# Kernel optimization log

Measured on AMD Instinct MI355X. Metric: run time of the kernel, lower is better.

## Reference

```python
import jax, jax.numpy as jnp
import numpy as np

GRID_SIZE = 5
SPLINE_ORDER = 3
GRID_RANGE = (-1.0, 1.0)
BATCH, IN_FEATURES, OUT_FEATURES = 8192, 512, 512


def make_grid():
    h = (GRID_RANGE[1] - GRID_RANGE[0]) / GRID_SIZE
    n = GRID_SIZE + 2 * SPLINE_ORDER + 1  # 12 knots
    return jnp.linspace(GRID_RANGE[0] - SPLINE_ORDER * h,
                        GRID_RANGE[1] + SPLINE_ORDER * h,
                        n, dtype=jnp.float32)


def b_spline(x, grid, k=SPLINE_ORDER):
    # Cox-de Boor recursion. x: (B, in) -> basis: (B, in, grid_size + k)
    x = x[..., None]                     # (B, in, 1)
    g = grid[None, None, :]              # (1, 1, n_knots)
    basis = ((x >= g[..., :-1]) & (x < g[..., 1:])).astype(x.dtype)
    for p in range(1, k + 1):
        left_denom = g[..., p:-1] - g[..., :-(p + 1)]
        right_denom = g[..., p + 1:] - g[..., 1:-p]
        left_denom = jnp.where(left_denom > 0, left_denom, jnp.ones_like(left_denom))
        right_denom = jnp.where(right_denom > 0, right_denom, jnp.ones_like(right_denom))
        left = (x - g[..., :-(p + 1)]) / left_denom * basis[..., :-1]
        right = (g[..., p + 1:] - x) / right_denom * basis[..., 1:]
        basis = left + right
    return basis


def setup_inputs() -> dict:
    key = jax.random.key(0)
    k1, k2, k3 = jax.random.split(key, 3)
    # x uniform in grid_range so spline basis is active
    x = jax.random.uniform(k1, (BATCH, IN_FEATURES), jnp.float32, minval=-1.0, maxval=1.0)
    # kaiming_uniform-like init for base weight
    bound = 1.0 / np.sqrt(IN_FEATURES)
    base_weight = jax.random.uniform(k2, (OUT_FEATURES, IN_FEATURES), jnp.float32,
                                     minval=-bound, maxval=bound)
    spline_weight = jax.random.normal(k3, (OUT_FEATURES, IN_FEATURES,
                                           GRID_SIZE + SPLINE_ORDER), jnp.float32) * 0.1
    return {"x": x, "base_weight": base_weight, "spline_weight": spline_weight}


def reference(x, base_weight, spline_weight):
    grid = make_grid()
    scale_base, scale_spline = 1.0, 1.0
    base_out = x @ base_weight.T                         # (B, out)
    basis = b_spline(x, grid, SPLINE_ORDER)              # (B, in, G+k)
    spline_out = jnp.einsum('bil,oil->bo', basis, spline_weight)
    return scale_base * base_out + scale_spline * spline_out
```

## Files before the change

### kernel.cpp

```cpp
#include <hip/hip_runtime.h>
#include <stdint.h>

typedef _Float16 half8 __attribute__((ext_vector_type(8)));
typedef float floatx4 __attribute__((ext_vector_type(4)));
typedef uint32_t u32x4 __attribute__((ext_vector_type(4)));

#define IF 512
#define NF 512
#define KT_TOTAL 72
#define TILE_B 16384
#define B_WS_BYTES ((size_t)KT_TOTAL * 4 * TILE_B)

__device__ __forceinline__ uint32_t swz(uint32_t b) {
  return b ^ (((b >> 7) & 7u) << 4);
}
__device__ __forceinline__ uint32_t pk(float a, float b) {
  return __builtin_bit_cast(uint32_t, __builtin_amdgcn_cvt_pkrtz(a, b));
}

__device__ __forceinline__ u32x4 BASIS8(float xv) {
  float u = (xv + 2.2f) * 2.5f;
  float fj = __builtin_floorf(u);
  fj = fminf(fmaxf(fj, 3.0f), 7.0f);
  float t = u - fj;
  float omt = 1.0f - t;
  float t2 = t * t, t3 = t2 * t;
  float w0 = omt * omt * omt * 0.16666666666666666f;
  float w1 = __builtin_fmaf(0.5f, t3, 0.66666666666666666f - t2);
  float w2 = __builtin_fmaf(0.5f, (t2 - t3) + t, 0.16666666666666666f);
  float w3 = t3 * 0.16666666666666666f;
  uint32_t c0 = pk(w0, w1);
  uint32_t c1 = pk(w2, w3);
  int j3 = (int)fj - 3;
  int sh = j3 << 4;
  uint64_t w = (uint64_t)c0 | ((uint64_t)c1 << 32);
  uint64_t lo = (sh < 64) ? (w << sh) : 0ull;
  uint64_t hi = (sh == 0) ? 0ull : ((sh < 64) ? (w >> (64 - sh)) : w);
  u32x4 r;
  r.x = (uint32_t)lo; r.y = (uint32_t)(lo >> 32);
  r.z = (uint32_t)hi; r.w = (uint32_t)(hi >> 32);
  return r;
}

__global__ __launch_bounds__(256)
void kan_zero(float4* __restrict__ p, int n4) {
  const int stride = gridDim.x * 256;
  for (int i = blockIdx.x * 256 + threadIdx.x; i < n4; i += stride)
    p[i] = (float4){0.f, 0.f, 0.f, 0.f};
}

__global__ __launch_bounds__(256)
void kan_prepB(const float* __restrict__ bwg, const float* __restrict__ swg,
               uint8_t* __restrict__ wsB)
{
  const int gid = blockIdx.x * 256 + threadIdx.x;
  const int T = gid >> 10;
  const int q = gid & 1023;
  const int kt = T >> 2;
  const int nt = T & 3;
  const uint32_t p = swz((uint32_t)q * 16u);
  const int row = p >> 7;
  const int c   = (p & 127) >> 1;
  const int n = nt * 128 + row;
  const float* src = (kt < 8) ? bwg + (size_t)n * IF + kt * 64 + c
                              : swg + (size_t)n * 4096 + (kt - 8) * 64 + c;
  float4 f0 = ((const float4*)src)[0];
  float4 f1 = ((const float4*)src)[1];
  u32x4 v; v.x = pk(f0.x, f0.y); v.y = pk(f0.z, f0.w);
           v.z = pk(f1.x, f1.y); v.w = pk(f1.z, f1.w);
  *(u32x4*)(wsB + (size_t)T * TILE_B + (size_t)q * 16) = v;
}

__global__ __launch_bounds__(256)
void kan_prepA(const float* __restrict__ xg, uint8_t* __restrict__ wsA, int row0)
{
  const int gid = blockIdx.x * 256 + threadIdx.x;
  const int bl = gid / 576;
  const int c  = gid - bl * 576;
  const int b  = row0 + bl;
  u32x4 v;
  if (c < 64) {
    const float* s = xg + (size_t)b * IF + c * 8;
    float4 f0 = ((const float4*)s)[0];
    float4 f1 = ((const float4*)s)[1];
    v.x = pk(f0.x, f0.y); v.y = pk(f0.z, f0.w);
    v.z = pk(f1.x, f1.y); v.w = pk(f1.z, f1.w);
  } else {
    v = BASIS8(xg[(size_t)b * IF + (c - 64)]);
  }
  const int mt = bl >> 7;
  const int r  = bl & 127;
  const int kt = c >> 3;
  const uint32_t lin = (uint32_t)r * 128u + (uint32_t)(c & 7) * 16u;
  *(u32x4*)(wsA + (size_t)(mt * KT_TOTAL + kt) * TILE_B + swz(lin)) = v;
}

__global__ __launch_bounds__(512, 4)
void kan_gemm(const uint8_t* __restrict__ wsA, const uint8_t* __restrict__ wsB,
              float* __restrict__ outg, int row0, int mtPerX)
{
  __shared__ _Float16 As[2][8192];
  __shared__ _Float16 Bs[2][8192];

  const int tid = threadIdx.x, lane = tid & 63, wv = tid >> 6;
  const int wm = wv >> 2, wn = wv & 3;

  const int bid = blockIdx.x;
  const int x = bid & 7;
  const int j = bid >> 3;
  const int kz  = j & 1;
  const int ntI = (j >> 1) & 3;
  const int mt  = x * mtPerX + (j >> 3);
  const int bm0 = row0 + mt * 128;
  const int bn0 = ntI * 128;
  const int kt0 = kz * 36, kt1 = kt0 + 36;

  char* AsB = (char*)As;
  char* BsB = (char*)Bs;

  uint32_t rdA[4], rdB[2];
  {
    const int rr = lane & 15;
    const uint32_t cc = (uint32_t)(lane >> 4) * 16u;
#pragma unroll
    for (int mi = 0; mi < 4; ++mi)
      rdA[mi] = swz((uint32_t)(wm * 64 + mi * 16 + rr) * 128u + cc);
#pragma unroll
    for (int ni = 0; ni < 2; ++ni)
      rdB[ni] = swz((uint32_t)(wn * 32 + ni * 16 + rr) * 128u + cc);
  }

  floatx4 acc[4][2];
#pragma unroll
  for (int mi = 0; mi < 4; ++mi)
#pragma unroll
    for (int ni = 0; ni < 2; ++ni)
      acc[mi][ni] = (floatx4){0.f, 0.f, 0.f, 0.f};

  auto STAGE = [&](int kt, int nb) {
    const uint8_t* sa = wsA + (size_t)(mt * KT_TOTAL + kt) * TILE_B + (size_t)tid * 16;
    const uint8_t* sb = wsB + (size_t)(kt * 4 + ntI) * TILE_B + (size_t)tid * 16;
    char* da = AsB + nb * TILE_B + tid * 16;
    char* db = BsB + nb * TILE_B + tid * 16;
    __builtin_amdgcn_global_load_lds((const __attribute__((address_space(1))) uint32_t*)sa,
                                     (__attribute__((address_space(3))) uint32_t*)da, 16, 0, 0);
    __builtin_amdgcn_global_load_lds((const __attribute__((address_space(1))) uint32_t*)(sa + 8192),
                                     (__attribute__((address_space(3))) uint32_t*)(da + 8192), 16, 0, 0);
    __builtin_amdgcn_global_load_lds((const __attribute__((address_space(1))) uint32_t*)sb,
                                     (__attribute__((address_space(3))) uint32_t*)db, 16, 0, 0);
    __builtin_amdgcn_global_load_lds((const __attribute__((address_space(1))) uint32_t*)(sb + 8192),
                                     (__attribute__((address_space(3))) uint32_t*)(db + 8192), 16, 0, 0);
  };

  auto COMPUTE = [&](int cb) {
    const char* ab = AsB + cb * TILE_B;
    const char* bb = BsB + cb * TILE_B;
#pragma unroll
    for (int kk = 0; kk < 2; ++kk) {
      const uint32_t ko = (uint32_t)(kk * 64);
      half8 a[4], b[2];
#pragma unroll
      for (int mi = 0; mi < 4; ++mi)
        a[mi] = *(const half8*)(ab + (rdA[mi] ^ ko));
#pragma unroll
      for (int ni = 0; ni < 2; ++ni)
        b[ni] = *(const half8*)(bb + (rdB[ni] ^ ko));
#pragma unroll
      for (int mi = 0; mi < 4; ++mi)
#pragma unroll
        for (int ni = 0; ni < 2; ++ni)
          acc[mi][ni] = __builtin_amdgcn_mfma_f32_16x16x32_f16(a[mi], b[ni], acc[mi][ni], 0, 0, 0);
    }
  };

  STAGE(kt0, 0);
  __syncthreads();
#pragma unroll 1
  for (int kt = kt0; kt < kt1; ++kt) {
    const int cur = (kt - kt0) & 1;
    if (kt + 1 < kt1) STAGE(kt + 1, cur ^ 1);
    COMPUTE(cur);
    __syncthreads();
  }

  const int er = (lane >> 4) * 4;
  const int ec = lane & 15;
#pragma unroll
  for (int mi = 0; mi < 4; ++mi) {
#pragma unroll
    for (int ni = 0; ni < 2; ++ni) {
      const size_t base = (size_t)(bm0 + wm * 64 + mi * 16 + er) * NF
                        + (size_t)(bn0 + wn * 32 + ni * 16 + ec);
#pragma unroll
      for (int e = 0; e < 4; ++e)
        unsafeAtomicAdd(outg + base + (size_t)e * NF, acc[mi][ni][e]);
    }
  }
}

extern "C" void kernel_launch(void* const* d_in, const int* in_sizes, int n_in,
                              void* d_out, int out_size, void* d_ws, size_t ws_size,
                              hipStream_t stream) {
  const float* x  = (const float*)d_in[0];
  const float* bw = (const float*)d_in[1];
  const float* sw = (const float*)d_in[2];
  float* out = (float*)d_out;
  uint8_t* wsB = (uint8_t*)d_ws;
  uint8_t* wsA = wsB + B_WS_BYTES;

  int R = 8192;
  while (R > 1024 && B_WS_BYTES + (size_t)R * 4608 * 2 > ws_size) R >>= 1;
  const int mtPerX = (R / 128) / 8;

  hipLaunchKernelGGL(kan_zero,  dim3(2048), dim3(256), 0, stream, (float4*)out, out_size / 4);
  hipLaunchKernelGGL(kan_prepB, dim3(1152), dim3(256), 0, stream, bw, sw, wsB);
  for (int r0 = 0; r0 < 8192; r0 += R) {
    hipLaunchKernelGGL(kan_prepA, dim3(R * 576 / 256), dim3(256), 0, stream, x, wsA, r0);
    hipLaunchKernelGGL(kan_gemm,  dim3(R / 16), dim3(512), 0, stream, wsA, wsB, out, r0, mtPerX);
  }
}
```

Measured before the change: 92.84 us.

## Fuse B-spline basis generation into GEMM A-fragments, drop A workspace

Removes the prepA kernel that materialized an fp16 A matrix (x plus spline bases) in workspace. The GEMM now builds A fragments directly in registers: it loads x (or a transposed copy from a new transpose kernel) and computes BASIS8 per MFMA fragment, so only B is staged through LDS. The block tile grows to 256x128 with 4x4 MFMA per wave and occupancy drops to 2 blocks per CU. This trades A-matrix HBM traffic and an extra launch for more register pressure and VALU basis work inside the GEMM loop.

```diff
diff --git a/kernel.cpp b/kernel.cpp
--- a/kernel.cpp
+++ b/kernel.cpp
@@ -7,9 +7,8 @@
 
 #define IF 512
 #define NF 512
-#define KT_TOTAL 72
 #define TILE_B 16384
-#define B_WS_BYTES ((size_t)KT_TOTAL * 4 * TILE_B)
+#define B_WS_BYTES ((size_t)72 * 4 * TILE_B)
 
 __device__ __forceinline__ uint32_t swz(uint32_t b) {
   return b ^ (((b >> 7) & 7u) << 4);
@@ -72,130 +71,169 @@
 }
 
 __global__ __launch_bounds__(256)
-void kan_prepA(const float* __restrict__ xg, uint8_t* __restrict__ wsA, int row0)
+void kan_xT(const float* __restrict__ xg, float* __restrict__ xTg)
 {
-  const int gid = blockIdx.x * 256 + threadIdx.x;
-  const int bl = gid / 576;
-  const int c  = gid - bl * 576;
-  const int b  = row0 + bl;
-  u32x4 v;
-  if (c < 64) {
-    const float* s = xg + (size_t)b * IF + c * 8;
-    float4 f0 = ((const float4*)s)[0];
-    float4 f1 = ((const float4*)s)[1];
-    v.x = pk(f0.x, f0.y); v.y = pk(f0.z, f0.w);
-    v.z = pk(f1.x, f1.y); v.w = pk(f1.z, f1.w);
-  } else {
-    v = BASIS8(xg[(size_t)b * IF + (c - 64)]);
-  }
-  const int mt = bl >> 7;
-  const int r  = bl & 127;
-  const int kt = c >> 3;
-  const uint32_t lin = (uint32_t)r * 128u + (uint32_t)(c & 7) * 16u;
-  *(u32x4*)(wsA + (size_t)(mt * KT_TOTAL + kt) * TILE_B + swz(lin)) = v;
-}
-
-__global__ __launch_bounds__(512, 4)
-void kan_gemm(const uint8_t* __restrict__ wsA, const uint8_t* __restrict__ wsB,
-              float* __restrict__ outg, int row0, int mtPerX)
+  __shared__ float t[64][65];
+  const int bi = blockIdx.x & 7;
+  const int bb = blockIdx.x >> 3;
+  const int li = threadIdx.x & 63, lr = threadIdx.x >> 6;
+#pragma unroll
+  for (int r = 0; r < 64; r += 4)
+    t[r + lr][li] = xg[(size_t)(bb * 64 + r + lr) * IF + bi * 64 + li];
+  __syncthreads();
+#pragma unroll
+  for (int r = 0; r < 64; r += 4)
+    xTg[(size_t)(bi * 64 + r + lr) * 8192 + bb * 64 + li] = t[li][r + lr];
+}
+
+#define STAGE(kt, nb) do { \
+    const uint8_t* sb_ = wsB + (size_t)((kt) * 4 + ntI) * TILE_B + (size_t)tid * 16; \
+    char* db_ = BsB + (nb) * TILE_B + tid * 16; \
+    __builtin_amdgcn_global_load_lds((const __attribute__((address_space(1))) uint32_t*)sb_, \
+                                     (__attribute__((address_space(3))) uint32_t*)db_, 16, 0, 0); \
+    __builtin_amdgcn_global_load_lds((const __attribute__((address_space(1))) uint32_t*)(sb_ + 8192), \
+                                     (__attribute__((address_space(3))) uint32_t*)(db_ + 8192), 16, 0, 0); \
+  } while (0)
+
+#define XLS(kt, xs) do { \
+    const int i0_ = ((kt) - 8) * 8; \
+    _Pragma("unroll") \
+    for (int mi = 0; mi < 4; ++mi) \
+      _Pragma("unroll") \
+      for (int kk = 0; kk < 2; ++kk) \
+        xs[mi * 2 + kk] = xTg[(size_t)(i0_ + kk * 4 + hi) * 8192 + rowbase + mi * 16]; \
+  } while (0)
+
+#define MAKEAS(xs, aF) do { \
+    _Pragma("unroll") \
+    for (int q = 0; q < 8; ++q) aF[q] = BASIS8(xs[q]); \
+  } while (0)
+
+#define XLB(kt, xf) do { \
+    _Pragma("unroll") \
+    for (int mi = 0; mi < 4; ++mi) \
+      _Pragma("unroll") \
+      for (int kk = 0; kk < 2; ++kk) { \
+        const float* s_ = xg + (size_t)(rowbase + mi * 16) * IF + (kt) * 64 + kk * 32 + hi * 8; \
+        xf[(mi * 2 + kk) * 2]     = ((const float4*)s_)[0]; \
+        xf[(mi * 2 + kk) * 2 + 1] = ((const float4*)s_)[1]; \
+      } \
+  } while (0)
+
+#define MAKEAB(xf, aF) do { \
+    _Pragma("unroll") \
+    for (int q = 0; q < 8; ++q) { \
+      u32x4 v_; \
+      v_.x = pk(xf[q * 2].x, xf[q * 2].y);     v_.y = pk(xf[q * 2].z, xf[q * 2].w); \
+      v_.z = pk(xf[q * 2 + 1].x, xf[q * 2 + 1].y); v_.w = pk(xf[q * 2 + 1].z, xf[q * 2 + 1].w); \
+      aF[q] = v_; \
+    } \
+  } while (0)
+
+#define COMPUTE(cb, aF) do { \
+    _Pragma("unroll") \
+    for (int kk = 0; kk < 2; ++kk) { \
+      u32x4 bF[4]; \
+      _Pragma("unroll") \
+      for (int ni = 0; ni < 4; ++ni) \
+        bF[ni] = *(const u32x4*)(BsB + (cb) * TILE_B + (rdB[ni] ^ (uint32_t)(kk * 64))); \
+      _Pragma("unroll") \
+      for (int mi = 0; mi < 4; ++mi) \
+        _Pragma("unroll") \
+        for (int ni = 0; ni < 4; ++ni) \
+          acc[mi][ni] = __builtin_amdgcn_mfma_f32_16x16x32_f16( \
+              __builtin_bit_cast(half8, aF[mi * 2 + kk]), \
+              __builtin_bit_cast(half8, bF[ni]), acc[mi][ni], 0, 0, 0); \
+    } \
+  } while (0)
+
+__global__ __launch_bounds__(512, 2)
+void kan_gemm(const float* __restrict__ xg, const float* __restrict__ xTg,
+              const uint8_t* __restrict__ wsB, float* __restrict__ outg)
 {
-  __shared__ _Float16 As[2][8192];
   __shared__ _Float16 Bs[2][8192];
+  char* BsB = (char*)Bs;
 
   const int tid = threadIdx.x, lane = tid & 63, wv = tid >> 6;
-  const int wm = wv >> 2, wn = wv & 3;
+  const int wm = wv >> 1, wn = wv & 1;
+  const int rr = lane & 15, hi = lane >> 4;
 
   const int bid = blockIdx.x;
-  const int x = bid & 7;
-  const int j = bid >> 3;
+  const int x = bid & 7, j = bid >> 3;
   const int kz  = j & 1;
   const int ntI = (j >> 1) & 3;
-  const int mt  = x * mtPerX + (j >> 3);
-  const int bm0 = row0 + mt * 128;
+  const int mt  = x * 4 + (j >> 3);
+  const int brow0 = mt * 256;
   const int bn0 = ntI * 128;
-  const int kt0 = kz * 36, kt1 = kt0 + 36;
-
-  char* AsB = (char*)As;
-  char* BsB = (char*)Bs;
-
-  uint32_t rdA[4], rdB[2];
-  {
-    const int rr = lane & 15;
-    const uint32_t cc = (uint32_t)(lane >> 4) * 16u;
-#pragma unroll
-    for (int mi = 0; mi < 4; ++mi)
-      rdA[mi] = swz((uint32_t)(wm * 64 + mi * 16 + rr) * 128u + cc);
-#pragma unroll
-    for (int ni = 0; ni < 2; ++ni)
-      rdB[ni] = swz((uint32_t)(wn * 32 + ni * 16 + rr) * 128u + cc);
+  const int kt0 = kz * 36;
+  const int rowbase = brow0 + wm * 64 + rr;
+
+  uint32_t rdB[4];
+#pragma unroll
+  for (int ni = 0; ni < 4; ++ni)
+    rdB[ni] = swz((uint32_t)(wn * 64 + ni * 16 + rr) * 128u + (uint32_t)hi * 16u);
+
+  floatx4 acc[4][4];
+#pragma unroll
+  for (int mi = 0; mi < 4; ++mi)
+#pragma unroll
+    for (int ni = 0; ni < 4; ++ni)
+      acc[mi][ni] = (floatx4){0.f, 0.f, 0.f, 0.f};
+
+  u32x4 aF0[8], aF1[8];
+  float xs0[8], xs1[8];
+
+  STAGE(kt0, 0);
+
+  if (kz == 0) {
+    float4 xf[16];
+    XLB(0, xf); MAKEAB(xf, aF0);
+    __syncthreads();
+#pragma unroll 1
+    for (int t = 0; t < 8; t += 2) {
+      STAGE(t + 1, 1);
+      if (t + 1 < 8) XLB(t + 1, xf);
+      COMPUTE(0, aF0);
+      if (t + 1 < 8) MAKEAB(xf, aF1);
+      __syncthreads();
+      STAGE(t + 2, 0);
+      if (t + 2 < 8) XLB(t + 2, xf);
+      COMPUTE(1, aF1);
+      if (t + 2 < 8) MAKEAB(xf, aF0);
+      __syncthreads();
+    }
+    XLS(8, xs0); MAKEAS(xs0, aF0);
+  } else {
+    XLS(36, xs0); MAKEAS(xs0, aF0);
+    __syncthreads();
   }
 
-  floatx4 acc[4][2];
+  const int sBeg = kz ? 36 : 8;
+  const int s1 = kt0 + 36;
+#pragma unroll 1
+  for (int kt = sBeg; kt < s1; kt += 2) {
+    STAGE(kt + 1, 1); XLS(kt + 1, xs1);
+    COMPUTE(0, aF0);
+    MAKEAS(xs1, aF1);
+    __syncthreads();
+    const bool more = (kt + 2) < s1;
+    if (more) { STAGE(kt + 2, 0); XLS(kt + 2, xs0); }
+    COMPUTE(1, aF1);
+    if (more) MAKEAS(xs0, aF0);
+    __syncthreads();
+  }
+
+  const int er = hi * 4, ec = rr;
 #pragma unroll
   for (int mi = 0; mi < 4; ++mi)
 #pragma unroll
-    for (int ni = 0; ni < 2; ++ni)
-      acc[mi][ni] = (floatx4){0.f, 0.f, 0.f, 0.f};
-
-  auto STAGE = [&](int kt, int nb) {
-    const uint8_t* sa = wsA + (size_t)(mt * KT_TOTAL + kt) * TILE_B + (size_t)tid * 16;
-    const uint8_t* sb = wsB + (size_t)(kt * 4 + ntI) * TILE_B + (size_t)tid * 16;
-    char* da = AsB + nb * TILE_B + tid * 16;
-    char* db = BsB + nb * TILE_B + tid * 16;
-    __builtin_amdgcn_global_load_lds((const __attribute__((address_space(1))) uint32_t*)sa,
-                                     (__attribute__((address_space(3))) uint32_t*)da, 16, 0, 0);
-    __builtin_amdgcn_global_load_lds((const __attribute__((address_space(1))) uint32_t*)(sa + 8192),
-                                     (__attribute__((address_space(3))) uint32_t*)(da + 8192), 16, 0, 0);
-    __builtin_amdgcn_global_load_lds((const __attribute__((address_space(1))) uint32_t*)sb,
-                                     (__attribute__((address_space(3))) uint32_t*)db, 16, 0, 0);
-    __builtin_amdgcn_global_load_lds((const __attribute__((address_space(1))) uint32_t*)(sb + 8192),
-                                     (__attribute__((address_space(3))) uint32_t*)(db + 8192), 16, 0, 0);
-  };
-
-  auto COMPUTE = [&](int cb) {
-    const char* ab = AsB + cb * TILE_B;
-    const char* bb = BsB + cb * TILE_B;
-#pragma unroll
-    for (int kk = 0; kk < 2; ++kk) {
-      const uint32_t ko = (uint32_t)(kk * 64);
-      half8 a[4], b[2];
-#pragma unroll
-      for (int mi = 0; mi < 4; ++mi)
-        a[mi] = *(const half8*)(ab + (rdA[mi] ^ ko));
-#pragma unroll
-      for (int ni = 0; ni < 2; ++ni)
-        b[ni] = *(const half8*)(bb + (rdB[ni] ^ ko));
-#pragma unroll
-      for (int mi = 0; mi < 4; ++mi)
-#pragma unroll
-        for (int ni = 0; ni < 2; ++ni)
-          acc[mi][ni] = __builtin_amdgcn_mfma_f32_16x16x32_f16(a[mi], b[ni], acc[mi][ni], 0, 0, 0);
-    }
-  };
-
-  STAGE(kt0, 0);
-  __syncthreads();
-#pragma unroll 1
-  for (int kt = kt0; kt < kt1; ++kt) {
-    const int cur = (kt - kt0) & 1;
-    if (kt + 1 < kt1) STAGE(kt + 1, cur ^ 1);
-    COMPUTE(cur);
-    __syncthreads();
-  }
-
-  const int er = (lane >> 4) * 4;
-  const int ec = lane & 15;
-#pragma unroll
-  for (int mi = 0; mi < 4; ++mi) {
-#pragma unroll
-    for (int ni = 0; ni < 2; ++ni) {
-      const size_t base = (size_t)(bm0 + wm * 64 + mi * 16 + er) * NF
-                        + (size_t)(bn0 + wn * 32 + ni * 16 + ec);
+    for (int ni = 0; ni < 4; ++ni) {
+      const size_t base = (size_t)(brow0 + wm * 64 + mi * 16 + er) * NF
+                        + (size_t)(bn0 + wn * 64 + ni * 16 + ec);
 #pragma unroll
       for (int e = 0; e < 4; ++e)
         unsafeAtomicAdd(outg + base + (size_t)e * NF, acc[mi][ni][e]);
     }
-  }
 }
 
 extern "C" void kernel_launch(void* const* d_in, const int* in_sizes, int n_in,
@@ -206,16 +244,10 @@
   const float* sw = (const float*)d_in[2];
   float* out = (float*)d_out;
   uint8_t* wsB = (uint8_t*)d_ws;
-  uint8_t* wsA = wsB + B_WS_BYTES;
-
-  int R = 8192;
-  while (R > 1024 && B_WS_BYTES + (size_t)R * 4608 * 2 > ws_size) R >>= 1;
-  const int mtPerX = (R / 128) / 8;
+  float*   xT  = (float*)(wsB + B_WS_BYTES);
 
   hipLaunchKernelGGL(kan_zero,  dim3(2048), dim3(256), 0, stream, (float4*)out, out_size / 4);
   hipLaunchKernelGGL(kan_prepB, dim3(1152), dim3(256), 0, stream, bw, sw, wsB);
-  for (int r0 = 0; r0 < 8192; r0 += R) {
-    hipLaunchKernelGGL(kan_prepA, dim3(R * 576 / 256), dim3(256), 0, stream, x, wsA, r0);
-    hipLaunchKernelGGL(kan_gemm,  dim3(R / 16), dim3(512), 0, stream, wsA, wsB, out, r0, mtPerX);
-  }
-}
+  hipLaunchKernelGGL(kan_xT,    dim3(1024), dim3(256), 0, stream, x, xT);
+  hipLaunchKernelGGL(kan_gemm,  dim3(256),  dim3(512), 0, stream, x, xT, wsB, out);
+}
```

Measured after the change: 114.5 us. +23.3%, slower.

## Fuse spline basis generation into GEMM and use 256-thread blocks with larger warp tiles

Applied to the files above, without the earlier changes.

The B-spline basis is no longer written to a large workspace by a separate prep kernel. The GEMM now loads x rows directly and computes the basis into LDS for the spline K-tiles, while the linear-x tiles still come from a small converted fp16 workspace. Blocks shrink to 256 threads, each wave covers a 64x64 output tile, and occupancy is raised to 2 blocks. The goal is to remove the roughly 75MB basis write and reread and the row chunking. The cost is that basis ALU work and LDS stores now sit inside the GEMM loop, and fewer waves per block may hide latency less well.

```diff
diff --git a/kernel.cpp b/kernel.cpp
--- a/kernel.cpp
+++ b/kernel.cpp
@@ -7,9 +7,9 @@
 
 #define IF 512
 #define NF 512
-#define KT_TOTAL 72
-#define TILE_B 16384
-#define B_WS_BYTES ((size_t)KT_TOTAL * 4 * TILE_B)
+#define TILE_BYTES 16384
+#define B_WS_BYTES ((size_t)72 * 4 * TILE_BYTES)
+#define XA_WS_BYTES ((size_t)64 * 8 * TILE_BYTES)
 
 __device__ __forceinline__ uint32_t swz(uint32_t b) {
   return b ^ (((b >> 7) & 7u) << 4);
@@ -68,134 +68,157 @@
   float4 f1 = ((const float4*)src)[1];
   u32x4 v; v.x = pk(f0.x, f0.y); v.y = pk(f0.z, f0.w);
            v.z = pk(f1.x, f1.y); v.w = pk(f1.z, f1.w);
-  *(u32x4*)(wsB + (size_t)T * TILE_B + (size_t)q * 16) = v;
+  *(u32x4*)(wsB + (size_t)T * TILE_BYTES + (size_t)q * 16) = v;
 }
 
 __global__ __launch_bounds__(256)
-void kan_prepA(const float* __restrict__ xg, uint8_t* __restrict__ wsA, int row0)
+void kan_prepXA(const float* __restrict__ xg, uint8_t* __restrict__ wsXA)
 {
   const int gid = blockIdx.x * 256 + threadIdx.x;
-  const int bl = gid / 576;
-  const int c  = gid - bl * 576;
-  const int b  = row0 + bl;
-  u32x4 v;
-  if (c < 64) {
-    const float* s = xg + (size_t)b * IF + c * 8;
-    float4 f0 = ((const float4*)s)[0];
-    float4 f1 = ((const float4*)s)[1];
-    v.x = pk(f0.x, f0.y); v.y = pk(f0.z, f0.w);
-    v.z = pk(f1.x, f1.y); v.w = pk(f1.z, f1.w);
-  } else {
-    v = BASIS8(xg[(size_t)b * IF + (c - 64)]);
-  }
-  const int mt = bl >> 7;
-  const int r  = bl & 127;
-  const int kt = c >> 3;
-  const uint32_t lin = (uint32_t)r * 128u + (uint32_t)(c & 7) * 16u;
-  *(u32x4*)(wsA + (size_t)(mt * KT_TOTAL + kt) * TILE_B + swz(lin)) = v;
-}
-
-__global__ __launch_bounds__(512, 4)
-void kan_gemm(const uint8_t* __restrict__ wsA, const uint8_t* __restrict__ wsB,
-              float* __restrict__ outg, int row0, int mtPerX)
+  const int T = gid >> 10;
+  const int q = gid & 1023;
+  const int mt = T >> 3;
+  const int kt = T & 7;
+  const uint32_t p = swz((uint32_t)q * 16u);
+  const int row = p >> 7;
+  const int c   = (p & 127) >> 1;
+  const float* src = xg + (size_t)(mt * 128 + row) * IF + kt * 64 + c;
+  float4 f0 = ((const float4*)src)[0];
+  float4 f1 = ((const float4*)src)[1];
+  u32x4 v; v.x = pk(f0.x, f0.y); v.y = pk(f0.z, f0.w);
+           v.z = pk(f1.x, f1.y); v.w = pk(f1.z, f1.w);
+  *(u32x4*)(wsXA + (size_t)T * TILE_BYTES + (size_t)q * 16) = v;
+}
+
+__global__ __launch_bounds__(256, 2)
+void kan_gemm(const float* __restrict__ xg, const uint8_t* __restrict__ wsB,
+              const uint8_t* __restrict__ wsXA, float* __restrict__ outg)
 {
   __shared__ _Float16 As[2][8192];
   __shared__ _Float16 Bs[2][8192];
+  char* AsB = (char*)As;
+  char* BsB = (char*)Bs;
 
   const int tid = threadIdx.x, lane = tid & 63, wv = tid >> 6;
-  const int wm = wv >> 2, wn = wv & 3;
+  const int wm = wv >> 1, wn = wv & 1;
+  const int rr = lane & 15, hi = lane >> 4;
 
   const int bid = blockIdx.x;
-  const int x = bid & 7;
-  const int j = bid >> 3;
+  const int x = bid & 7, j = bid >> 3;
   const int kz  = j & 1;
   const int ntI = (j >> 1) & 3;
-  const int mt  = x * mtPerX + (j >> 3);
-  const int bm0 = row0 + mt * 128;
-  const int bn0 = ntI * 128;
+  const int mt  = x * 8 + (j >> 3);
+  const int bm0 = mt * 128, bn0 = ntI * 128;
   const int kt0 = kz * 36, kt1 = kt0 + 36;
 
-  char* AsB = (char*)As;
-  char* BsB = (char*)Bs;
-
-  uint32_t rdA[4], rdB[2];
-  {
-    const int rr = lane & 15;
-    const uint32_t cc = (uint32_t)(lane >> 4) * 16u;
-#pragma unroll
-    for (int mi = 0; mi < 4; ++mi)
-      rdA[mi] = swz((uint32_t)(wm * 64 + mi * 16 + rr) * 128u + cc);
-#pragma unroll
-    for (int ni = 0; ni < 2; ++ni)
-      rdB[ni] = swz((uint32_t)(wn * 32 + ni * 16 + rr) * 128u + cc);
-  }
-
-  floatx4 acc[4][2];
+  const int rT = tid >> 1;
+  const int il = (tid & 1) * 4;
+  uint32_t wA[4];
+#pragma unroll
+  for (int jj = 0; jj < 4; ++jj)
+    wA[jj] = swz((uint32_t)rT * 128u + (uint32_t)(il + jj) * 16u);
+
+  uint32_t rdA[4], rdB[4];
 #pragma unroll
   for (int mi = 0; mi < 4; ++mi)
-#pragma unroll
-    for (int ni = 0; ni < 2; ++ni)
+    rdA[mi] = swz((uint32_t)(wm * 64 + mi * 16 + rr) * 128u + (uint32_t)hi * 16u);
+#pragma unroll
+  for (int ni = 0; ni < 4; ++ni)
+    rdB[ni] = swz((uint32_t)(wn * 64 + ni * 16 + rr) * 128u + (uint32_t)hi * 16u);
+
+  floatx4 acc[4][4];
+#pragma unroll
+  for (int mi = 0; mi < 4; ++mi)
+#pragma unroll
+    for (int ni = 0; ni < 4; ++ni)
       acc[mi][ni] = (floatx4){0.f, 0.f, 0.f, 0.f};
 
-  auto STAGE = [&](int kt, int nb) {
-    const uint8_t* sa = wsA + (size_t)(mt * KT_TOTAL + kt) * TILE_B + (size_t)tid * 16;
-    const uint8_t* sb = wsB + (size_t)(kt * 4 + ntI) * TILE_B + (size_t)tid * 16;
-    char* da = AsB + nb * TILE_B + tid * 16;
-    char* db = BsB + nb * TILE_B + tid * 16;
-    __builtin_amdgcn_global_load_lds((const __attribute__((address_space(1))) uint32_t*)sa,
-                                     (__attribute__((address_space(3))) uint32_t*)da, 16, 0, 0);
-    __builtin_amdgcn_global_load_lds((const __attribute__((address_space(1))) uint32_t*)(sa + 8192),
-                                     (__attribute__((address_space(3))) uint32_t*)(da + 8192), 16, 0, 0);
-    __builtin_amdgcn_global_load_lds((const __attribute__((address_space(1))) uint32_t*)sb,
-                                     (__attribute__((address_space(3))) uint32_t*)db, 16, 0, 0);
-    __builtin_amdgcn_global_load_lds((const __attribute__((address_space(1))) uint32_t*)(sb + 8192),
-                                     (__attribute__((address_space(3))) uint32_t*)(db + 8192), 16, 0, 0);
-  };
-
+  auto STAGE_B = [&](int kt, int nb) {
+    const uint8_t* s = wsB + (size_t)(kt * 4 + ntI) * TILE_BYTES + (size_t)tid * 16;
+    char* d = BsB + nb * TILE_BYTES + tid * 16;
+#pragma unroll
+    for (int q = 0; q < 4; ++q)
+      __builtin_amdgcn_global_load_lds(
+          (const __attribute__((address_space(1))) uint32_t*)(s + q * 4096),
+          (__attribute__((address_space(3))) uint32_t*)(d + q * 4096), 16, 0, 0);
+  };
+  auto STAGE_AI = [&](int kt, int nb) {
+    const uint8_t* s = wsXA + (size_t)(mt * 8 + kt) * TILE_BYTES + (size_t)tid * 16;
+    char* d = AsB + nb * TILE_BYTES + tid * 16;
+#pragma unroll
+    for (int q = 0; q < 4; ++q)
+      __builtin_amdgcn_global_load_lds(
+          (const __attribute__((address_space(1))) uint32_t*)(s + q * 4096),
+          (__attribute__((address_space(3))) uint32_t*)(d + q * 4096), 16, 0, 0);
+  };
+  auto XL = [&](int kt) -> float4 {
+    return *(const float4*)(xg + (size_t)(bm0 + rT) * IF + (kt - 8) * 8 + il);
+  };
+  auto WRITEA = [&](float4 xq, int nb) {
+    char* base = AsB + nb * TILE_BYTES;
+    *(u32x4*)(base + wA[0]) = BASIS8(xq.x);
+    *(u32x4*)(base + wA[1]) = BASIS8(xq.y);
+    *(u32x4*)(base + wA[2]) = BASIS8(xq.z);
+    *(u32x4*)(base + wA[3]) = BASIS8(xq.w);
+  };
   auto COMPUTE = [&](int cb) {
-    const char* ab = AsB + cb * TILE_B;
-    const char* bb = BsB + cb * TILE_B;
+    const char* ab = AsB + cb * TILE_BYTES;
+    const char* bb = BsB + cb * TILE_BYTES;
 #pragma unroll
     for (int kk = 0; kk < 2; ++kk) {
       const uint32_t ko = (uint32_t)(kk * 64);
-      half8 a[4], b[2];
+      half8 a[4], b[4];
 #pragma unroll
       for (int mi = 0; mi < 4; ++mi)
         a[mi] = *(const half8*)(ab + (rdA[mi] ^ ko));
 #pragma unroll
-      for (int ni = 0; ni < 2; ++ni)
+      for (int ni = 0; ni < 4; ++ni)
         b[ni] = *(const half8*)(bb + (rdB[ni] ^ ko));
 #pragma unroll
       for (int mi = 0; mi < 4; ++mi)
 #pragma unroll
-        for (int ni = 0; ni < 2; ++ni)
+        for (int ni = 0; ni < 4; ++ni)
           acc[mi][ni] = __builtin_amdgcn_mfma_f32_16x16x32_f16(a[mi], b[ni], acc[mi][ni], 0, 0, 0);
     }
   };
 
-  STAGE(kt0, 0);
+  STAGE_B(kt0, 0);
+  if (kz == 0) {
+    STAGE_AI(0, 0);
+  } else {
+    float4 xq = XL(kt0);
+    WRITEA(xq, 0);
+  }
   __syncthreads();
+
 #pragma unroll 1
   for (int kt = kt0; kt < kt1; ++kt) {
     const int cur = (kt - kt0) & 1;
-    if (kt + 1 < kt1) STAGE(kt + 1, cur ^ 1);
+    const int nxt = cur ^ 1;
+    const bool more = (kt + 1) < kt1;
+    float4 xq;
+    bool spl = false;
+    if (more) {
+      STAGE_B(kt + 1, nxt);
+      if (kt + 1 < 8) STAGE_AI(kt + 1, nxt);
+      else { xq = XL(kt + 1); spl = true; }
+    }
     COMPUTE(cur);
+    if (spl) WRITEA(xq, nxt);
     __syncthreads();
   }
 
-  const int er = (lane >> 4) * 4;
-  const int ec = lane & 15;
-#pragma unroll
-  for (int mi = 0; mi < 4; ++mi) {
-#pragma unroll
-    for (int ni = 0; ni < 2; ++ni) {
+  const int er = hi * 4, ec = rr;
+#pragma unroll
+  for (int mi = 0; mi < 4; ++mi)
+#pragma unroll
+    for (int ni = 0; ni < 4; ++ni) {
       const size_t base = (size_t)(bm0 + wm * 64 + mi * 16 + er) * NF
-                        + (size_t)(bn0 + wn * 32 + ni * 16 + ec);
+                        + (size_t)(bn0 + wn * 64 + ni * 16 + ec);
 #pragma unroll
       for (int e = 0; e < 4; ++e)
         unsafeAtomicAdd(outg + base + (size_t)e * NF, acc[mi][ni][e]);
     }
-  }
 }
 
 extern "C" void kernel_launch(void* const* d_in, const int* in_sizes, int n_in,
@@ -205,17 +228,11 @@
   const float* bw = (const float*)d_in[1];
   const float* sw = (const float*)d_in[2];
   float* out = (float*)d_out;
-  uint8_t* wsB = (uint8_t*)d_ws;
-  uint8_t* wsA = wsB + B_WS_BYTES;
-
-  int R = 8192;
-  while (R > 1024 && B_WS_BYTES + (size_t)R * 4608 * 2 > ws_size) R >>= 1;
-  const int mtPerX = (R / 128) / 8;
-
-  hipLaunchKernelGGL(kan_zero,  dim3(2048), dim3(256), 0, stream, (float4*)out, out_size / 4);
-  hipLaunchKernelGGL(kan_prepB, dim3(1152), dim3(256), 0, stream, bw, sw, wsB);
-  for (int r0 = 0; r0 < 8192; r0 += R) {
-    hipLaunchKernelGGL(kan_prepA, dim3(R * 576 / 256), dim3(256), 0, stream, x, wsA, r0);
-    hipLaunchKernelGGL(kan_gemm,  dim3(R / 16), dim3(512), 0, stream, wsA, wsB, out, r0, mtPerX);
-  }
-}
+  uint8_t* wsB  = (uint8_t*)d_ws;
+  uint8_t* wsXA = wsB + B_WS_BYTES;
+
+  hipLaunchKernelGGL(kan_zero,   dim3(2048), dim3(256), 0, stream, (float4*)out, out_size / 4);
+  hipLaunchKernelGGL(kan_prepB,  dim3(1152), dim3(256), 0, stream, bw, sw, wsB);
+  hipLaunchKernelGGL(kan_prepXA, dim3(2048), dim3(256), 0, stream, x, wsXA);
+  hipLaunchKernelGGL(kan_gemm,   dim3(512),  dim3(256), 0, stream, x, wsB, wsXA, out);
+}
```

Measured after the change: 92.92 us. Within noise of the previous version (+0.1%).
